# Performance work log

Measured on AMD Instinct MI355X. Metric: run time of the kernel, lower is better.

Reference implementation:

```python
import jax, jax.numpy as jnp
import numpy as np

DIM = 64
HEADS = 8
WIN = (8, 8)  # window_num


def setup_inputs() -> dict:
    key = jax.random.key(0)
    ks = jax.random.split(key, 6)
    b, c, H, W = 16, DIM, 256, 256
    n = WIN[0] * WIN[1]
    x = jax.random.normal(ks[0], (b, c, H, W), dtype=jnp.float32)
    w_qkv = jax.random.normal(ks[1], (3 * c, c), dtype=jnp.float32) * (1.0 / np.sqrt(c))
    w_dw = jax.random.normal(ks[2], (3 * c, 1, 3, 3), dtype=jnp.float32) * (1.0 / 3.0)
    w_proj = jax.random.normal(ks[3], (c, c), dtype=jnp.float32) * (1.0 / np.sqrt(c))
    b_proj = jnp.zeros((c,), dtype=jnp.float32)
    # trunc_normal_(std=1) approximated by clipped normal for the reference baseline
    pos_emb = jnp.clip(jax.random.normal(ks[4], (1, HEADS, n, n), dtype=jnp.float32), -2.0, 2.0)
    return {"x": x, "w_qkv": w_qkv, "w_dw": w_dw, "w_proj": w_proj,
            "b_proj": b_proj, "pos_emb": pos_emb}


def _to_window_tokens(t, n0, n1, heads):
    # t: [b, c, n0*b0, n1*b1] -> [b, heads, n0*n1, (b0*b1*c)//heads]
    b, c, H, W = t.shape
    b0, b1 = H // n0, W // n1
    t = t.reshape(b, c, n0, b0, n1, b1)
    t = t.transpose(0, 2, 4, 3, 5, 1)            # b n0 n1 b0 b1 c
    t = t.reshape(b, n0 * n1, b0 * b1 * c)       # b n (b0 b1 c)
    d = (b0 * b1 * c) // heads
    return t.reshape(b, n0 * n1, heads, d).transpose(0, 2, 1, 3)  # b h n d


def _from_window_tokens(t, n0, n1, b0, b1, c):
    # t: [b, heads, n, d] -> [b, c, n0*b0, n1*b1]
    b = t.shape[0]
    t = t.transpose(0, 2, 1, 3).reshape(b, n0 * n1, b0 * b1 * c)  # b n (h d)
    t = t.reshape(b, n0, n1, b0, b1, c)
    t = t.transpose(0, 5, 1, 3, 2, 4)            # b c n0 b0 n1 b1
    return t.reshape(b, c, n0 * b0, n1 * b1)


def reference(x, w_qkv, w_dw, w_proj, b_proj, pos_emb):
    b, c, H, W = x.shape
    n0, n1 = WIN
    b0, b1 = H // n0, W // n1
    # 1x1 pointwise qkv projection (no bias)
    qkv = jnp.einsum('bchw,oc->bohw', x, w_qkv)
    # 3x3 depthwise conv, padding=1, groups=3c, no bias
    qkv = jax.lax.conv_general_dilated(
        qkv, w_dw, window_strides=(1, 1), padding=((1, 1), (1, 1)),
        feature_group_count=3 * c,
        dimension_numbers=('NCHW', 'OIHW', 'NCHW'))
    q, k, v = jnp.split(qkv, 3, axis=1)
    q = _to_window_tokens(q, n0, n1, HEADS)
    k = _to_window_tokens(k, n0, n1, HEADS)
    v = _to_window_tokens(v, n0, n1, HEADS)
    head_dim = b0 * b1 * c / HEADS
    scale = head_dim ** (-0.5)
    sim = jnp.einsum('bhid,bhjd->bhij', q * scale, k) + pos_emb
    attn = jax.nn.softmax(sim, axis=-1)
    out = jnp.einsum('bhij,bhjd->bhid', attn, v)
    out = _from_window_tokens(out, n0, n1, b0, b1, c)
    # 1x1 projection with bias
    out = jnp.einsum('bchw,oc->bohw', out, w_proj) + b_proj[None, :, None, None]
    return out
```

## Files before the change

kernel.cpp:

```cpp
#include <hip/hip_runtime.h>
#include <hip/hip_bf16.h>

typedef __hip_bfloat16 bf16;
typedef unsigned int u32;
typedef __attribute__((ext_vector_type(8))) short bf16x8;
typedef __attribute__((ext_vector_type(4))) float f32x4;

#define HWSZ 65536u

__device__ __forceinline__ float b2f_lo(u32 w){ return __uint_as_float(w << 16); }
__device__ __forceinline__ float b2f_hi(u32 w){ return __uint_as_float(w & 0xffff0000u); }
__device__ __forceinline__ float b2f(bf16 v){ return __bfloat162float(v); }
__device__ __forceinline__ bf16 f2b(float v){ return __float2bfloat16(v); }

__device__ __forceinline__ u32 f2bbits(float f){
  u32 x = __float_as_uint(f);
  return ((x + 0x7fffu + ((x >> 16) & 1u)) >> 16) & 0xffffu;
}

__device__ __forceinline__ void unpack8(uint4 v, float* f){
  f[0]=b2f_lo(v.x); f[1]=b2f_hi(v.x);
  f[2]=b2f_lo(v.y); f[3]=b2f_hi(v.y);
  f[4]=b2f_lo(v.z); f[5]=b2f_hi(v.z);
  f[6]=b2f_lo(v.w); f[7]=b2f_hi(v.w);
}

union ABu { u32 u[4]; bf16x8 v; uint4 q; };

__device__ __forceinline__ int xsw(int c8, int px){
  return c8 * 192 + ((px & ~7) | ((px ^ c8) & 7));
}

__global__ __launch_bounds__(512, 6) void k12_fused(
    const float* __restrict__ x, const float* __restrict__ wq,
    const float* __restrict__ wdw, bf16* __restrict__ tok){
  __shared__ uint4 xs[8 * 192];
  __shared__ unsigned short qs[192 * 68];
  int t = threadIdx.x;
  int lane = t & 63, w = t >> 6;
  int r16 = lane & 15, g4 = lane >> 4;

  u32 n = blockIdx.x;
  u32 bid = (n & 7u) * 1024u + (n >> 3);
  u32 xt = bid & 31u, yt = (bid >> 5) & 15u, b = bid >> 9;
  int y0 = (int)yt * 16, x0 = (int)xt * 8;

  const float* xb = x + (size_t)b * 64 * HWSZ;

  for (int u = t; u < 576; u += 512){
    int jq = u & 3, rr = (u >> 2) % 18, c8 = u / 72;
    int yy = y0 - 1 + rr;
    float va[2][10];
    if ((u32)yy < 256u){
      #pragma unroll
      for (int jc = 0; jc < 2; jc++){
        const float* p = xb + (size_t)(c8 * 8 + jq * 2 + jc) * HWSZ + ((size_t)yy << 8);
        float4 A  = *(const float4*)(p + x0);
        float4 Bq = *(const float4*)(p + x0 + 4);
        va[jc][0] = (x0 > 0) ? p[x0 - 1] : 0.f;
        va[jc][1] = A.x;  va[jc][2] = A.y;  va[jc][3] = A.z;  va[jc][4] = A.w;
        va[jc][5] = Bq.x; va[jc][6] = Bq.y; va[jc][7] = Bq.z; va[jc][8] = Bq.w;
        va[jc][9] = (x0 + 8 < 256) ? p[x0 + 8] : 0.f;
      }
    } else {
      #pragma unroll
      for (int jc = 0; jc < 2; jc++)
        #pragma unroll
        for (int e = 0; e < 10; e++) va[jc][e] = 0.f;
    }
    #pragma unroll
    for (int e = 0; e < 10; e++){
      u32 wv = f2bbits(va[0][e]) | (f2bbits(va[1][e]) << 16);
      ((u32*)&xs[xsw(c8, rr * 10 + e)])[jq] = wv;
    }
  }
  if (t < 96){
    int c8 = t / 12, px = 180 + (t % 12);
    xs[xsw(c8, px)] = make_uint4(0u, 0u, 0u, 0u);
  }

  int cth = lane, rp = w;
  int ot = w & 3, nh = w >> 2;
  u32 win = (yt >> 1) * 8u + (xt >> 2);

  for (int g = 0; g < 3; g++){
    __syncthreads();
    bf16x8 af[2];
    {
      int och = g * 64 + ot * 16 + r16;
      #pragma unroll
      for (int kt = 0; kt < 2; kt++){
        const float* wr = wq + och * 64 + kt * 32 + g4 * 8;
        ABu pk;
        #pragma unroll
        for (int j = 0; j < 4; j++)
          pk.u[j] = f2bbits(wr[2 * j]) | (f2bbits(wr[2 * j + 1]) << 16);
        af[kt] = pk.v;
      }
    }
    #pragma unroll
    for (int nt2 = 0; nt2 < 6; nt2++){
      int nt = nh * 6 + nt2;
      f32x4 acc = (f32x4){0.f, 0.f, 0.f, 0.f};
      #pragma unroll
      for (int kt = 0; kt < 2; kt++){
        uint4 uq = xs[xsw(kt * 4 + g4, nt * 16 + r16)];
        acc = __builtin_amdgcn_mfma_f32_16x16x32_bf16(
            af[kt], *reinterpret_cast<bf16x8*>(&uq), acc, 0, 0, 0);
      }
      int px = nt * 16 + r16;
      u32 lo = f2bbits(acc[0]) | (f2bbits(acc[1]) << 16);
      u32 hi = f2bbits(acc[2]) | (f2bbits(acc[3]) << 16);
      *(uint2*)&qs[px * 68 + ot * 16 + g4 * 4] = make_uint2(lo, hi);
    }
    __syncthreads();

    const float* wg = wdw + ((size_t)g * 64 + cth) * 9;
    float d0=wg[0],d1=wg[1],d2=wg[2],d3=wg[3],d4=wg[4],d5=wg[5],d6=wg[6],d7=wg[7],d8=wg[8];
    float rbf[4][10];
    #define QLD(s, R) do{ _Pragma("unroll") for (int _cr = 0; _cr < 10; _cr++) \
      rbf[s][_cr] = __uint_as_float(((u32)qs[((R) * 10 + _cr) * 68 + cth]) << 16); }while(0)
    QLD(0, rp * 2 + 0);
    QLD(1, rp * 2 + 1);
    QLD(2, rp * 2 + 2);
    QLD(3, rp * 2 + 3);
    #undef QLD
    #pragma unroll
    for (int rr2 = 0; rr2 < 2; rr2++){
      int r = rp * 2 + rr2;
      int h = (int)(yt & 1u) * 4 + (r >> 2);
      bf16* op = tok + (((((size_t)g * 16 + b) * 8 + h) * 64 + win) * 8192)
               + (size_t)(r & 3) * 2048 + (size_t)(xt & 3u) * 512 + cth;
      #pragma unroll
      for (int co = 0; co < 8; co++){
        float o = rbf[rr2][co]    * d0 + rbf[rr2][co + 1]    * d1 + rbf[rr2][co + 2]    * d2
                + rbf[rr2 + 1][co]* d3 + rbf[rr2 + 1][co + 1]* d4 + rbf[rr2 + 1][co + 2]* d5
                + rbf[rr2 + 2][co]* d6 + rbf[rr2 + 2][co + 1]* d7 + rbf[rr2 + 2][co + 2]* d8;
        op[co * 64] = f2b(o);
      }
    }
  }
}

__global__ __launch_bounds__(256) void k3_sim(
    const bf16* __restrict__ tok, float* __restrict__ sim4){
  __shared__ short qs[64 * 72];
  __shared__ short ks[64 * 72];
  int t = threadIdx.x;
  int lane = t & 63, w = t >> 6;
  int r16 = lane & 15, g4 = lane >> 4;
  u32 bid = blockIdx.x;
  u32 part = bid & 3u, h = (bid >> 2) & 7u, b = bid >> 5;
  const bf16* qb = tok + ((size_t)(((0 * 16 + b) * 8 + h) * 64)) * 8192 + part * 2048;
  const bf16* kb = tok + ((size_t)(((1 * 16 + b) * 8 + h) * 64)) * 8192 + part * 2048;

  int stok = t >> 2, soct = t & 3;

  f32x4 acc[4];
  #pragma unroll
  for (int jt = 0; jt < 4; jt++) acc[jt] = (f32x4){0.f,0.f,0.f,0.f};

  for (int s = 0; s < 32; s++){
    int d0 = s * 64;
    __syncthreads();
    {
      uint4 q0 = *(const uint4*)(qb + (size_t)stok * 8192 + d0 + soct * 8);
      uint4 q1 = *(const uint4*)(qb + (size_t)stok * 8192 + d0 + soct * 8 + 32);
      uint4 k0 = *(const uint4*)(kb + (size_t)stok * 8192 + d0 + soct * 8);
      uint4 k1 = *(const uint4*)(kb + (size_t)stok * 8192 + d0 + soct * 8 + 32);
      *(uint4*)&qs[stok * 72 + soct * 8]      = q0;
      *(uint4*)&qs[stok * 72 + soct * 8 + 32] = q1;
      *(uint4*)&ks[stok * 72 + soct * 8]      = k0;
      *(uint4*)&ks[stok * 72 + soct * 8 + 32] = k1;
    }
    __syncthreads();
    #pragma unroll
    for (int kt = 0; kt < 2; kt++){
      bf16x8 a = *(const bf16x8*)&qs[(w * 16 + r16) * 72 + kt * 32 + g4 * 8];
      #pragma unroll
      for (int jt = 0; jt < 4; jt++){
        bf16x8 bb = *(const bf16x8*)&ks[(jt * 16 + r16) * 72 + kt * 32 + g4 * 8];
        acc[jt] = __builtin_amdgcn_mfma_f32_16x16x32_bf16(a, bb, acc[jt], 0, 0, 0);
      }
    }
  }

  float* sp = sim4 + ((((size_t)part * 16 + b) * 8 + h) * 64) * 64;
  #pragma unroll
  for (int jt = 0; jt < 4; jt++)
    #pragma unroll
    for (int r = 0; r < 4; r++)
      sp[(w * 16 + g4 * 4 + r) * 64 + jt * 16 + r16] = acc[jt][r];
}

__global__ __launch_bounds__(64) void k4_softmax(
    const float* __restrict__ sim4, const float* __restrict__ pos, float* __restrict__ attn){
  int j = threadIdx.x;
  u32 bid = blockIdx.x;
  u32 i = bid & 63u, h = (bid >> 6) & 7u, b = bid >> 9;
  size_t o = (((size_t)b * 8 + h) * 64 + i) * 64 + j;
  const size_t pstride = (size_t)16 * 8 * 64 * 64;
  float s = sim4[o] + sim4[o + pstride] + sim4[o + 2 * pstride] + sim4[o + 3 * pstride];
  s = s * 0.011048543456039806f + pos[(((size_t)h * 64) + i) * 64 + j];
  float m = s;
  #pragma unroll
  for (int off = 32; off; off >>= 1) m = fmaxf(m, __shfl_xor(m, off));
  float e = __expf(s - m);
  float sum = e;
  #pragma unroll
  for (int off = 32; off; off >>= 1) sum += __shfl_xor(sum, off);
  attn[o] = e / sum;
}

__global__ __launch_bounds__(256) void k5_av(
    const bf16* __restrict__ tok, const float* __restrict__ attn, bf16* __restrict__ otok){
  __shared__ short vt[4][64 * 72];
  int t = threadIdx.x;
  int lane = t & 63, w = t >> 6;
  int r16 = lane & 15, g4 = lane >> 4;
  u32 bid = blockIdx.x;
  u32 q = bid & 3u, h = (bid >> 2) & 7u, b = bid >> 5;
  const bf16* vb = tok + ((size_t)(((2 * 16 + b) * 8 + h) * 64)) * 8192;
  const float* ab = attn + (((size_t)b * 8 + h) * 64) * 64;
  bf16* ob = otok + (((size_t)b * 8 + h) * 64) * 8192;

  bf16x8 af[4][2];
  #pragma unroll
  for (int it = 0; it < 4; it++)
    #pragma unroll
    for (int kt = 0; kt < 2; kt++){
      const float* ar = ab + (it * 16 + r16) * 64 + kt * 32 + g4 * 8;
      ABu pk;
      #pragma unroll
      for (int j = 0; j < 4; j++)
        pk.u[j] = f2bbits(ar[2 * j]) | (f2bbits(ar[2 * j + 1]) << 16);
      af[it][kt] = pk.v;
    }

  short* vtw = vt[w];
  for (int s = 0; s < 8; s++){
    int d0 = (int)q * 2048 + s * 256 + w * 64;
    uint4 ld[8];
    const bf16* vp = vb + (size_t)lane * 8192 + d0;
    #pragma unroll
    for (int u = 0; u < 8; u++) ld[u] = *(const uint4*)(vp + u * 8);
    #pragma unroll
    for (int u = 0; u < 8; u++){
      const u32* wd = (const u32*)&ld[u];
      #pragma unroll
      for (int e = 0; e < 4; e++){
        int d = u * 8 + e * 2;
        vtw[d * 72 + lane]       = (short)(wd[e] & 0xffffu);
        vtw[(d + 1) * 72 + lane] = (short)(wd[e] >> 16);
      }
    }
    #pragma unroll
    for (int dt = 0; dt < 4; dt++){
      bf16x8 b0 = *(const bf16x8*)&vtw[(dt * 16 + r16) * 72 + 0 * 32 + g4 * 8];
      bf16x8 b1 = *(const bf16x8*)&vtw[(dt * 16 + r16) * 72 + 1 * 32 + g4 * 8];
      #pragma unroll
      for (int it = 0; it < 4; it++){
        f32x4 acc = (f32x4){0.f,0.f,0.f,0.f};
        acc = __builtin_amdgcn_mfma_f32_16x16x32_bf16(af[it][0], b0, acc, 0, 0, 0);
        acc = __builtin_amdgcn_mfma_f32_16x16x32_bf16(af[it][1], b1, acc, 0, 0, 0);
        #pragma unroll
        for (int r = 0; r < 4; r++)
          ob[(size_t)(it * 16 + g4 * 4 + r) * 8192 + d0 + dt * 16 + r16] = f2b(acc[r]);
      }
    }
  }
}

__global__ __launch_bounds__(256) void k6_mfma(
    const bf16* __restrict__ otok, const float* __restrict__ wp,
    const float* __restrict__ bp, float* __restrict__ out){
  __shared__ uint4 xs[1024];
  int t = threadIdx.x;
  int lane = t & 63, w = t >> 6;
  u32 pix0 = blockIdx.x * 128u;
  u32 b = pix0 >> 16, hw0 = pix0 & 65535u;
  int y = (int)(hw0 >> 8);
  int p0 = y & 31, h = p0 >> 2, prow = (p0 & 3) * 2048;
  int iy = (y >> 5) << 3;

  {
    int pix = t & 127, half = t >> 7;
    int xx = (int)(hw0 & 255u) + pix;
    int i = iy + (xx >> 5), p1 = xx & 31;
    const bf16* ip = otok + ((((size_t)b * 8 + h) * 64 + i)) * 8192 + prow + p1 * 64;
    #pragma unroll
    for (int g = 0; g < 4; g++){
      int c8 = half * 4 + g;
      xs[c8 * 128 + pix] = *(const uint4*)(ip + c8 * 8);
    }
  }

  int r16 = lane & 15, g4 = lane >> 4;
  bf16x8 af[2];
  int och = w * 16 + r16;
  #pragma unroll
  for (int kt = 0; kt < 2; kt++){
    const float* wr = wp + och * 64 + kt * 32 + g4 * 8;
    ABu pk;
    #pragma unroll
    for (int j = 0; j < 4; j++)
      pk.u[j] = f2bbits(wr[2 * j]) | (f2bbits(wr[2 * j + 1]) << 16);
    af[kt] = pk.v;
  }
  float bias[4];
  #pragma unroll
  for (int r = 0; r < 4; r++) bias[r] = bp[w * 16 + g4 * 4 + r];
  __syncthreads();

  f32x4 acc[8];
  #pragma unroll
  for (int pt = 0; pt < 8; pt++) acc[pt] = (f32x4){bias[0], bias[1], bias[2], bias[3]};

  #pragma unroll
  for (int pt = 0; pt < 8; pt++){
    uint4 u0 = xs[(0 * 4 + g4) * 128 + pt * 16 + r16];
    uint4 u1 = xs[(1 * 4 + g4) * 128 + pt * 16 + r16];
    bf16x8 b0 = *reinterpret_cast<bf16x8*>(&u0);
    bf16x8 b1 = *reinterpret_cast<bf16x8*>(&u1);
    acc[pt] = __builtin_amdgcn_mfma_f32_16x16x32_bf16(af[0], b0, acc[pt], 0, 0, 0);
    acc[pt] = __builtin_amdgcn_mfma_f32_16x16x32_bf16(af[1], b1, acc[pt], 0, 0, 0);
  }

  float* op = out + (size_t)b * 64 * HWSZ + hw0;
  int ochb = w * 16 + g4 * 4;
  #pragma unroll
  for (int pt = 0; pt < 8; pt++)
    #pragma unroll
    for (int r = 0; r < 4; r++)
      op[(size_t)(ochb + r) * HWSZ + pt * 16 + r16] = acc[pt][r];
}

extern "C" void kernel_launch(void* const* d_in, const int* in_sizes, int n_in,
                              void* d_out, int out_size, void* d_ws, size_t ws_size,
                              hipStream_t stream){
  const float* x   = (const float*)d_in[0];
  const float* wq  = (const float*)d_in[1];
  const float* wdw = (const float*)d_in[2];
  const float* wp  = (const float*)d_in[3];
  const float* bp  = (const float*)d_in[4];
  const float* pos = (const float*)d_in[5];
  float* out = (float*)d_out;
  (void)in_sizes; (void)n_in; (void)out_size; (void)ws_size;

  char* ws = (char*)d_ws;
  bf16*  tok  = (bf16*)(ws + 402653184u);
  bf16*  otok = (bf16*)ws;
  float* sim4 = (float*)(ws + 134217728u);
  float* attn = (float*)(ws + 142606336u);

  k12_fused<<<dim3(8192), dim3(512), 0, stream>>>(x, wq, wdw, tok);
  k3_sim<<<dim3(512),   dim3(256), 0, stream>>>(tok, sim4);
  k4_softmax<<<dim3(8192), dim3(64), 0, stream>>>(sim4, pos, attn);
  k5_av<<<dim3(512),  dim3(256), 0, stream>>>(tok, attn, otok);
  k6_mfma<<<dim3(8192), dim3(256), 0, stream>>>(otok, wp, bp, out);
}
```

Baseline: 549.6 us.

## Hoist weight loads and repartition depthwise conv to channel pairs in fused QKV kernel

Loads and converts the pointwise QKV weights and all depthwise 3x3 weights once into registers before the three-group loop, instead of reloading them for each group. Repartitions the depthwise stage so each thread handles two adjacent channels and four columns with 32-bit shared loads and packed bf16x2 stores, replacing per-channel 16-bit loads and stores. Uses a rolling three-row register buffer. Drops the occupancy hint from the launch bounds, and the extra preloaded weights increase register pressure, which may lower occupancy.

```diff
diff --git a/kernel.cpp b/kernel.cpp
--- a/kernel.cpp
+++ b/kernel.cpp
@@ -31,7 +31,7 @@
   return c8 * 192 + ((px & ~7) | ((px ^ c8) & 7));
 }
 
-__global__ __launch_bounds__(512, 6) void k12_fused(
+__global__ __launch_bounds__(512) void k12_fused(
     const float* __restrict__ x, const float* __restrict__ wq,
     const float* __restrict__ wdw, bf16* __restrict__ tok){
   __shared__ uint4 xs[8 * 192];
@@ -46,6 +46,34 @@
   int y0 = (int)yt * 16, x0 = (int)xt * 8;
 
   const float* xb = x + (size_t)b * 64 * HWSZ;
+  int ot = w & 3, nh = w >> 2;
+
+  bf16x8 af[3][2];
+  #pragma unroll
+  for (int g = 0; g < 3; g++){
+    int och = g * 64 + ot * 16 + r16;
+    #pragma unroll
+    for (int kt = 0; kt < 2; kt++){
+      const float* wr = wq + och * 64 + kt * 32 + g4 * 8;
+      ABu pk;
+      #pragma unroll
+      for (int j = 0; j < 4; j++)
+        pk.u[j] = f2bbits(wr[2 * j]) | (f2bbits(wr[2 * j + 1]) << 16);
+      af[g][kt] = pk.v;
+    }
+  }
+
+  int c2 = t & 31, rq = (t >> 5) & 7, colh = t >> 8;
+  int r0 = rq * 2, cb = colh * 4;
+  float wA[3][9];
+  float wB[3][9];
+  #pragma unroll
+  for (int g = 0; g < 3; g++){
+    const float* wg = wdw + ((size_t)g * 64 + c2 * 2) * 9;
+    #pragma unroll
+    for (int k = 0; k < 9; k++){ wA[g][k] = wg[k]; wB[g][k] = wg[9 + k]; }
+  }
+  u32 win = (yt >> 1) * 8u + (xt >> 2);
 
   for (int u = t; u < 576; u += 512){
     int jq = u & 3, rr = (u >> 2) % 18, c8 = u / 72;
@@ -79,25 +107,8 @@
     xs[xsw(c8, px)] = make_uint4(0u, 0u, 0u, 0u);
   }
 
-  int cth = lane, rp = w;
-  int ot = w & 3, nh = w >> 2;
-  u32 win = (yt >> 1) * 8u + (xt >> 2);
-
   for (int g = 0; g < 3; g++){
     __syncthreads();
-    bf16x8 af[2];
-    {
-      int och = g * 64 + ot * 16 + r16;
-      #pragma unroll
-      for (int kt = 0; kt < 2; kt++){
-        const float* wr = wq + och * 64 + kt * 32 + g4 * 8;
-        ABu pk;
-        #pragma unroll
-        for (int j = 0; j < 4; j++)
-          pk.u[j] = f2bbits(wr[2 * j]) | (f2bbits(wr[2 * j + 1]) << 16);
-        af[kt] = pk.v;
-      }
-    }
     #pragma unroll
     for (int nt2 = 0; nt2 < 6; nt2++){
       int nt = nh * 6 + nt2;
@@ -106,7 +117,7 @@
       for (int kt = 0; kt < 2; kt++){
         uint4 uq = xs[xsw(kt * 4 + g4, nt * 16 + r16)];
         acc = __builtin_amdgcn_mfma_f32_16x16x32_bf16(
-            af[kt], *reinterpret_cast<bf16x8*>(&uq), acc, 0, 0, 0);
+            af[g][kt], *reinterpret_cast<bf16x8*>(&uq), acc, 0, 0, 0);
       }
       int px = nt * 16 + r16;
       u32 lo = f2bbits(acc[0]) | (f2bbits(acc[1]) << 16);
@@ -115,30 +126,35 @@
     }
     __syncthreads();
 
-    const float* wg = wdw + ((size_t)g * 64 + cth) * 9;
-    float d0=wg[0],d1=wg[1],d2=wg[2],d3=wg[3],d4=wg[4],d5=wg[5],d6=wg[6],d7=wg[7],d8=wg[8];
-    float rbf[4][10];
-    #define QLD(s, R) do{ _Pragma("unroll") for (int _cr = 0; _cr < 10; _cr++) \
-      rbf[s][_cr] = __uint_as_float(((u32)qs[((R) * 10 + _cr) * 68 + cth]) << 16); }while(0)
-    QLD(0, rp * 2 + 0);
-    QLD(1, rp * 2 + 1);
-    QLD(2, rp * 2 + 2);
-    QLD(3, rp * 2 + 3);
-    #undef QLD
+    const char* qbase = (const char*)qs + c2 * 4;
+    float fA[3][6], fB[3][6];
+    #define LDQ(s, RR) do{ _Pragma("unroll") for (int _cr = 0; _cr < 6; _cr++){ \
+      u32 _v = *(const u32*)(qbase + (size_t)(((RR) * 10 + cb + _cr)) * 136);   \
+      fA[s][_cr] = b2f_lo(_v); fB[s][_cr] = b2f_hi(_v); } }while(0)
+    LDQ(0, r0 + 0);
+    LDQ(1, r0 + 1);
+    LDQ(2, r0 + 2);
+
     #pragma unroll
     for (int rr2 = 0; rr2 < 2; rr2++){
-      int r = rp * 2 + rr2;
+      int r = r0 + rr2;
+      const int s0 = rr2 % 3, s1 = (rr2 + 1) % 3, s2 = (rr2 + 2) % 3;
       int h = (int)(yt & 1u) * 4 + (r >> 2);
       bf16* op = tok + (((((size_t)g * 16 + b) * 8 + h) * 64 + win) * 8192)
-               + (size_t)(r & 3) * 2048 + (size_t)(xt & 3u) * 512 + cth;
-      #pragma unroll
-      for (int co = 0; co < 8; co++){
-        float o = rbf[rr2][co]    * d0 + rbf[rr2][co + 1]    * d1 + rbf[rr2][co + 2]    * d2
-                + rbf[rr2 + 1][co]* d3 + rbf[rr2 + 1][co + 1]* d4 + rbf[rr2 + 1][co + 2]* d5
-                + rbf[rr2 + 2][co]* d6 + rbf[rr2 + 2][co + 1]* d7 + rbf[rr2 + 2][co + 2]* d8;
-        op[co * 64] = f2b(o);
-      }
-    }
+               + (size_t)(r & 3) * 2048 + (size_t)(xt & 3u) * 512 + (size_t)c2 * 2;
+      #pragma unroll
+      for (int j = 0; j < 4; j++){
+        float aA = fA[s0][j]*wA[g][0] + fA[s0][j+1]*wA[g][1] + fA[s0][j+2]*wA[g][2]
+                 + fA[s1][j]*wA[g][3] + fA[s1][j+1]*wA[g][4] + fA[s1][j+2]*wA[g][5]
+                 + fA[s2][j]*wA[g][6] + fA[s2][j+1]*wA[g][7] + fA[s2][j+2]*wA[g][8];
+        float aB = fB[s0][j]*wB[g][0] + fB[s0][j+1]*wB[g][1] + fB[s0][j+2]*wB[g][2]
+                 + fB[s1][j]*wB[g][3] + fB[s1][j+1]*wB[g][4] + fB[s1][j+2]*wB[g][5]
+                 + fB[s2][j]*wB[g][6] + fB[s2][j+1]*wB[g][7] + fB[s2][j+2]*wB[g][8];
+        *(u32*)(op + (cb + j) * 64) = f2bbits(aA) | (f2bbits(aB) << 16);
+      }
+      if (rr2 == 0) LDQ(s0, r0 + 3);
+    }
+    #undef LDQ
   }
 }
 
```

Result: slower. 662.8 us (+20.6%).

## Fold depthwise 3x3 into pointwise weights and compute conv as MFMA GEMM

Applied to the files above, without the earlier changes.

Precomputes combined weights w3[och][tap][c] = wdw*wq in a small pre-kernel, so the 1x1 projection followed by the depthwise 3x3 becomes a single implicit GEMM over K = 9 taps × 64 channels, computed directly with MFMA from the staged input tile. This removes the intermediate bf16 qs shared buffer, the extra syncs and the scalar depthwise FMA loop, and writes token outputs straight from the accumulators. In exchange it does 9x the MFMA work for the projection, holds 96 accumulator registers per thread with 256-thread blocks, and rounds the folded weights to bf16, which changes numerics slightly.

```diff
diff --git a/kernel.cpp b/kernel.cpp
--- a/kernel.cpp
+++ b/kernel.cpp
@@ -18,24 +18,23 @@
   return ((x + 0x7fffu + ((x >> 16) & 1u)) >> 16) & 0xffffu;
 }
 
-__device__ __forceinline__ void unpack8(uint4 v, float* f){
-  f[0]=b2f_lo(v.x); f[1]=b2f_hi(v.x);
-  f[2]=b2f_lo(v.y); f[3]=b2f_hi(v.y);
-  f[4]=b2f_lo(v.z); f[5]=b2f_hi(v.z);
-  f[6]=b2f_lo(v.w); f[7]=b2f_hi(v.w);
-}
-
 union ABu { u32 u[4]; bf16x8 v; uint4 q; };
 
 __device__ __forceinline__ int xsw(int c8, int px){
   return c8 * 192 + ((px & ~7) | ((px ^ c8) & 7));
 }
 
-__global__ __launch_bounds__(512, 6) void k12_fused(
-    const float* __restrict__ x, const float* __restrict__ wq,
-    const float* __restrict__ wdw, bf16* __restrict__ tok){
+__global__ __launch_bounds__(256) void k0_w3(
+    const float* __restrict__ wq, const float* __restrict__ wdw, bf16* __restrict__ w3){
+  int idx = blockIdx.x * 256 + threadIdx.x;
+  int och = idx / 576, r = idx - och * 576;
+  int tap = r >> 6, c = r & 63;
+  w3[idx] = f2b(wdw[och * 9 + tap] * wq[och * 64 + c]);
+}
+
+__global__ __launch_bounds__(256) void k12_fused(
+    const float* __restrict__ x, const bf16* __restrict__ w3, bf16* __restrict__ tok){
   __shared__ uint4 xs[8 * 192];
-  __shared__ unsigned short qs[192 * 68];
   int t = threadIdx.x;
   int lane = t & 63, w = t >> 6;
   int r16 = lane & 15, g4 = lane >> 4;
@@ -44,10 +43,9 @@
   u32 bid = (n & 7u) * 1024u + (n >> 3);
   u32 xt = bid & 31u, yt = (bid >> 5) & 15u, b = bid >> 9;
   int y0 = (int)yt * 16, x0 = (int)xt * 8;
-
   const float* xb = x + (size_t)b * 64 * HWSZ;
 
-  for (int u = t; u < 576; u += 512){
+  for (int u = t; u < 576; u += 256){
     int jq = u & 3, rr = (u >> 2) % 18, c8 = u / 72;
     int yy = y0 - 1 + rr;
     float va[2][10];
@@ -74,70 +72,57 @@
       ((u32*)&xs[xsw(c8, rr * 10 + e)])[jq] = wv;
     }
   }
-  if (t < 96){
-    int c8 = t / 12, px = 180 + (t % 12);
-    xs[xsw(c8, px)] = make_uint4(0u, 0u, 0u, 0u);
-  }
-
-  int cth = lane, rp = w;
-  int ot = w & 3, nh = w >> 2;
+  __syncthreads();
+
+  f32x4 acc[3][8];
+  #pragma unroll
+  for (int m = 0; m < 3; m++)
+    #pragma unroll
+    for (int nt = 0; nt < 8; nt++) acc[m][nt] = (f32x4){0.f, 0.f, 0.f, 0.f};
+
+  const bf16* w3r0 = w3 + (size_t)(16 * w + r16) * 576 + g4 * 8;
+  const bf16* w3r1 = w3r0 + (size_t)64 * 576;
+  const bf16* w3r2 = w3r1 + (size_t)64 * 576;
+
+  int orow = r16 >> 3, ocol = (r16 & 7) + 1;
+
+  #pragma unroll 2
+  for (int ks = 0; ks < 18; ks++){
+    int tap = ks >> 1;
+    int dy = tap / 3, dx = tap % 3;
+    ABu a0, a1, a2;
+    a0.q = *(const uint4*)(w3r0 + ks * 32);
+    a1.q = *(const uint4*)(w3r1 + ks * 32);
+    a2.q = *(const uint4*)(w3r2 + ks * 32);
+    int c8 = (ks & 1) * 4 + g4;
+    int prow = orow + dy;
+    int pcol = ocol + dx - 1;
+    #pragma unroll
+    for (int nt = 0; nt < 8; nt++){
+      int px = (2 * nt + prow) * 10 + pcol;
+      uint4 uq = xs[xsw(c8, px)];
+      bf16x8 bv = *reinterpret_cast<bf16x8*>(&uq);
+      acc[0][nt] = __builtin_amdgcn_mfma_f32_16x16x32_bf16(a0.v, bv, acc[0][nt], 0, 0, 0);
+      acc[1][nt] = __builtin_amdgcn_mfma_f32_16x16x32_bf16(a1.v, bv, acc[1][nt], 0, 0, 0);
+      acc[2][nt] = __builtin_amdgcn_mfma_f32_16x16x32_bf16(a2.v, bv, acc[2][nt], 0, 0, 0);
+    }
+  }
+
   u32 win = (yt >> 1) * 8u + (xt >> 2);
-
-  for (int g = 0; g < 3; g++){
-    __syncthreads();
-    bf16x8 af[2];
-    {
-      int och = g * 64 + ot * 16 + r16;
-      #pragma unroll
-      for (int kt = 0; kt < 2; kt++){
-        const float* wr = wq + och * 64 + kt * 32 + g4 * 8;
-        ABu pk;
-        #pragma unroll
-        for (int j = 0; j < 4; j++)
-          pk.u[j] = f2bbits(wr[2 * j]) | (f2bbits(wr[2 * j + 1]) << 16);
-        af[kt] = pk.v;
-      }
-    }
-    #pragma unroll
-    for (int nt2 = 0; nt2 < 6; nt2++){
-      int nt = nh * 6 + nt2;
-      f32x4 acc = (f32x4){0.f, 0.f, 0.f, 0.f};
-      #pragma unroll
-      for (int kt = 0; kt < 2; kt++){
-        uint4 uq = xs[xsw(kt * 4 + g4, nt * 16 + r16)];
-        acc = __builtin_amdgcn_mfma_f32_16x16x32_bf16(
-            af[kt], *reinterpret_cast<bf16x8*>(&uq), acc, 0, 0, 0);
-      }
-      int px = nt * 16 + r16;
-      u32 lo = f2bbits(acc[0]) | (f2bbits(acc[1]) << 16);
-      u32 hi = f2bbits(acc[2]) | (f2bbits(acc[3]) << 16);
-      *(uint2*)&qs[px * 68 + ot * 16 + g4 * 4] = make_uint2(lo, hi);
-    }
-    __syncthreads();
-
-    const float* wg = wdw + ((size_t)g * 64 + cth) * 9;
-    float d0=wg[0],d1=wg[1],d2=wg[2],d3=wg[3],d4=wg[4],d5=wg[5],d6=wg[6],d7=wg[7],d8=wg[8];
-    float rbf[4][10];
-    #define QLD(s, R) do{ _Pragma("unroll") for (int _cr = 0; _cr < 10; _cr++) \
-      rbf[s][_cr] = __uint_as_float(((u32)qs[((R) * 10 + _cr) * 68 + cth]) << 16); }while(0)
-    QLD(0, rp * 2 + 0);
-    QLD(1, rp * 2 + 1);
-    QLD(2, rp * 2 + 2);
-    QLD(3, rp * 2 + 3);
-    #undef QLD
-    #pragma unroll
-    for (int rr2 = 0; rr2 < 2; rr2++){
-      int r = rp * 2 + rr2;
-      int h = (int)(yt & 1u) * 4 + (r >> 2);
-      bf16* op = tok + (((((size_t)g * 16 + b) * 8 + h) * 64 + win) * 8192)
-               + (size_t)(r & 3) * 2048 + (size_t)(xt & 3u) * 512 + cth;
-      #pragma unroll
-      for (int co = 0; co < 8; co++){
-        float o = rbf[rr2][co]    * d0 + rbf[rr2][co + 1]    * d1 + rbf[rr2][co + 2]    * d2
-                + rbf[rr2 + 1][co]* d3 + rbf[rr2 + 1][co + 1]* d4 + rbf[rr2 + 1][co + 2]* d5
-                + rbf[rr2 + 2][co]* d6 + rbf[rr2 + 2][co + 1]* d7 + rbf[rr2 + 2][co + 2]* d8;
-        op[co * 64] = f2b(o);
-      }
+  int choff = w * 16 + g4 * 4;
+  int p1 = (int)(xt & 3u) * 8 + (r16 & 7);
+  #pragma unroll
+  for (int m = 0; m < 3; m++){
+    #pragma unroll
+    for (int nt = 0; nt < 8; nt++){
+      int row = 2 * nt + orow;
+      int h = (int)(yt & 1u) * 4 + (row >> 2);
+      int p0r = row & 3;
+      size_t off = (((((size_t)m * 16 + b) * 8 + h) * 64 + win) * 8192)
+                 + (size_t)p0r * 2048 + (size_t)p1 * 64 + choff;
+      u32 lo = f2bbits(acc[m][nt][0]) | (f2bbits(acc[m][nt][1]) << 16);
+      u32 hi = f2bbits(acc[m][nt][2]) | (f2bbits(acc[m][nt][3]) << 16);
+      *(uint2*)(tok + off) = make_uint2(lo, hi);
     }
   }
 }
@@ -352,8 +337,10 @@
   bf16*  otok = (bf16*)ws;
   float* sim4 = (float*)(ws + 134217728u);
   float* attn = (float*)(ws + 142606336u);
-
-  k12_fused<<<dim3(8192), dim3(512), 0, stream>>>(x, wq, wdw, tok);
+  bf16*  w3   = (bf16*)(ws + 144703488u);
+
+  k0_w3<<<dim3(432), dim3(256), 0, stream>>>(wq, wdw, w3);
+  k12_fused<<<dim3(8192), dim3(256), 0, stream>>>(x, w3, tok);
   k3_sim<<<dim3(512),   dim3(256), 0, stream>>>(tok, sim4);
   k4_softmax<<<dim3(8192), dim3(64), 0, stream>>>(sim4, pos, attn);
   k5_av<<<dim3(512),  dim3(256), 0, stream>>>(tok, attn, otok);
```

New measurement: 672.8 us. 22.4% more time.

## Shrink fused qkv+dwconv tile to 8x8 pixels with 256-thread blocks

Applied to the files above, without the earlier changes.

Halves the spatial tile of the fused pointwise-projection and depthwise-conv kernel from 16x8 to 8x8 output pixels. Blocks drop from 512 to 256 threads and the grid doubles. Each wave now computes all 7 pixel tiles for its own 16 output channels, and the halo loader uses 160 threads handling 4 channels each. This cuts shared memory per block so more blocks can be resident, but the 1-pixel halo is a larger fraction of each tile, so more redundant loads and MFMA work are done.

```diff
diff --git a/kernel.cpp b/kernel.cpp
--- a/kernel.cpp
+++ b/kernel.cpp
@@ -28,33 +28,34 @@
 union ABu { u32 u[4]; bf16x8 v; uint4 q; };
 
 __device__ __forceinline__ int xsw(int c8, int px){
-  return c8 * 192 + ((px & ~7) | ((px ^ c8) & 7));
-}
-
-__global__ __launch_bounds__(512, 6) void k12_fused(
+  return c8 * 112 + ((px & ~7) | ((px ^ c8) & 7));
+}
+
+__global__ __launch_bounds__(256) void k12_fused(
     const float* __restrict__ x, const float* __restrict__ wq,
     const float* __restrict__ wdw, bf16* __restrict__ tok){
-  __shared__ uint4 xs[8 * 192];
-  __shared__ unsigned short qs[192 * 68];
+  __shared__ uint4 xs[8 * 112];
+  __shared__ unsigned short qs[112 * 68];
   int t = threadIdx.x;
   int lane = t & 63, w = t >> 6;
   int r16 = lane & 15, g4 = lane >> 4;
 
   u32 n = blockIdx.x;
-  u32 bid = (n & 7u) * 1024u + (n >> 3);
-  u32 xt = bid & 31u, yt = (bid >> 5) & 15u, b = bid >> 9;
-  int y0 = (int)yt * 16, x0 = (int)xt * 8;
+  u32 bid = (n & 7u) * 2048u + (n >> 3);
+  u32 xt = bid & 31u, yt = (bid >> 5) & 31u, b = bid >> 10;
+  int y0 = (int)yt * 8, x0 = (int)xt * 8;
 
   const float* xb = x + (size_t)b * 64 * HWSZ;
 
-  for (int u = t; u < 576; u += 512){
-    int jq = u & 3, rr = (u >> 2) % 18, c8 = u / 72;
+  if (t < 160){
+    int u = t;
+    int jh = u & 1, rr = (u >> 1) % 10, c8 = u / 20;
     int yy = y0 - 1 + rr;
-    float va[2][10];
+    float va[4][10];
     if ((u32)yy < 256u){
       #pragma unroll
-      for (int jc = 0; jc < 2; jc++){
-        const float* p = xb + (size_t)(c8 * 8 + jq * 2 + jc) * HWSZ + ((size_t)yy << 8);
+      for (int jc = 0; jc < 4; jc++){
+        const float* p = xb + (size_t)(c8 * 8 + jh * 4 + jc) * HWSZ + ((size_t)yy << 8);
         float4 A  = *(const float4*)(p + x0);
         float4 Bq = *(const float4*)(p + x0 + 4);
         va[jc][0] = (x0 > 0) ? p[x0 - 1] : 0.f;
@@ -64,30 +65,30 @@
       }
     } else {
       #pragma unroll
-      for (int jc = 0; jc < 2; jc++)
+      for (int jc = 0; jc < 4; jc++)
         #pragma unroll
         for (int e = 0; e < 10; e++) va[jc][e] = 0.f;
     }
     #pragma unroll
     for (int e = 0; e < 10; e++){
-      u32 wv = f2bbits(va[0][e]) | (f2bbits(va[1][e]) << 16);
-      ((u32*)&xs[xsw(c8, rr * 10 + e)])[jq] = wv;
+      u32 w0 = f2bbits(va[0][e]) | (f2bbits(va[1][e]) << 16);
+      u32 w1 = f2bbits(va[2][e]) | (f2bbits(va[3][e]) << 16);
+      ((uint2*)&xs[xsw(c8, rr * 10 + e)])[jh] = make_uint2(w0, w1);
     }
   }
   if (t < 96){
-    int c8 = t / 12, px = 180 + (t % 12);
+    int c8 = t / 12, px = 100 + (t % 12);
     xs[xsw(c8, px)] = make_uint4(0u, 0u, 0u, 0u);
   }
 
-  int cth = lane, rp = w;
-  int ot = w & 3, nh = w >> 2;
-  u32 win = (yt >> 1) * 8u + (xt >> 2);
+  int cth = t & 63, rq = w;
+  u32 win = (yt >> 2) * 8u + (xt >> 2);
 
   for (int g = 0; g < 3; g++){
     __syncthreads();
     bf16x8 af[2];
     {
-      int och = g * 64 + ot * 16 + r16;
+      int och = g * 64 + w * 16 + r16;
       #pragma unroll
       for (int kt = 0; kt < 2; kt++){
         const float* wr = wq + och * 64 + kt * 32 + g4 * 8;
@@ -99,8 +100,7 @@
       }
     }
     #pragma unroll
-    for (int nt2 = 0; nt2 < 6; nt2++){
-      int nt = nh * 6 + nt2;
+    for (int nt = 0; nt < 7; nt++){
       f32x4 acc = (f32x4){0.f, 0.f, 0.f, 0.f};
       #pragma unroll
       for (int kt = 0; kt < 2; kt++){
@@ -111,7 +111,7 @@
       int px = nt * 16 + r16;
       u32 lo = f2bbits(acc[0]) | (f2bbits(acc[1]) << 16);
       u32 hi = f2bbits(acc[2]) | (f2bbits(acc[3]) << 16);
-      *(uint2*)&qs[px * 68 + ot * 16 + g4 * 4] = make_uint2(lo, hi);
+      *(uint2*)&qs[px * 68 + w * 16 + g4 * 4] = make_uint2(lo, hi);
     }
     __syncthreads();
 
@@ -120,17 +120,17 @@
     float rbf[4][10];
     #define QLD(s, R) do{ _Pragma("unroll") for (int _cr = 0; _cr < 10; _cr++) \
       rbf[s][_cr] = __uint_as_float(((u32)qs[((R) * 10 + _cr) * 68 + cth]) << 16); }while(0)
-    QLD(0, rp * 2 + 0);
-    QLD(1, rp * 2 + 1);
-    QLD(2, rp * 2 + 2);
-    QLD(3, rp * 2 + 3);
+    QLD(0, rq * 2 + 0);
+    QLD(1, rq * 2 + 1);
+    QLD(2, rq * 2 + 2);
+    QLD(3, rq * 2 + 3);
     #undef QLD
     #pragma unroll
     for (int rr2 = 0; rr2 < 2; rr2++){
-      int r = rp * 2 + rr2;
-      int h = (int)(yt & 1u) * 4 + (r >> 2);
+      int r = rq * 2 + rr2;
+      int h = (int)(yt & 3u) * 2 + (r >> 2);
       bf16* op = tok + (((((size_t)g * 16 + b) * 8 + h) * 64 + win) * 8192)
-               + (size_t)(r & 3) * 2048 + (size_t)(xt & 3u) * 512 + cth;
+               + (size_t)(r & 3) * 2048 + (size_t)((xt & 3u) * 8) * 64 + cth;
       #pragma unroll
       for (int co = 0; co < 8; co++){
         float o = rbf[rr2][co]    * d0 + rbf[rr2][co + 1]    * d1 + rbf[rr2][co + 2]    * d2
@@ -353,7 +353,7 @@
   float* sim4 = (float*)(ws + 134217728u);
   float* attn = (float*)(ws + 142606336u);
 
-  k12_fused<<<dim3(8192), dim3(512), 0, stream>>>(x, wq, wdw, tok);
+  k12_fused<<<dim3(16384), dim3(256), 0, stream>>>(x, wq, wdw, tok);
   k3_sim<<<dim3(512),   dim3(256), 0, stream>>>(tok, sim4);
   k4_softmax<<<dim3(8192), dim3(64), 0, stream>>>(sim4, pos, attn);
   k5_av<<<dim3(512),  dim3(256), 0, stream>>>(tok, attn, otok);
```

Measured after the change: 554.5 us. About the same (+0.9%).
